# Kernel optimization log

Hardware: AMD Instinct MI355X
Metric: run time of the kernel (lower is better)

The kernel has to match this reference:

```python
import jax, jax.numpy as jnp
import numpy as np

EMBED_DIM = 768
ATTN_DIM = 64


def setup_inputs() -> dict:
    key = jax.random.key(0)
    k1, k2, k3, k4 = jax.random.split(key, 4)
    embedded = jax.random.normal(k1, (4, 4096, EMBED_DIM), dtype=jnp.float32)
    # nn.Linear(embed, attn, bias=False).weight has shape [attn, embed]; y = x @ W.T
    scale = 1.0 / np.sqrt(EMBED_DIM)
    Wq = jax.random.uniform(k2, (ATTN_DIM, EMBED_DIM), dtype=jnp.float32, minval=-scale, maxval=scale)
    Wk = jax.random.uniform(k3, (ATTN_DIM, EMBED_DIM), dtype=jnp.float32, minval=-scale, maxval=scale)
    Wv = jax.random.uniform(k4, (ATTN_DIM, EMBED_DIM), dtype=jnp.float32, minval=-scale, maxval=scale)
    return {"embedded": embedded, "Wq": Wq, "Wk": Wk, "Wv": Wv}


def reference(embedded, Wq, Wk, Wv):
    # Q, K, V: [b, s, a]
    Q = jnp.einsum('bse,ae->bsa', embedded, Wq)
    K = jnp.einsum('bse,ae->bsa', embedded, Wk)
    V = jnp.einsum('bse,ae->bsa', embedded, Wv)
    attn_dim = K.shape[2]
    scores = jnp.einsum('bqa,bka->bqk', Q, K) / jnp.sqrt(jnp.float32(attn_dim))
    s = scores.shape[1]
    # causal mask: positions above the diagonal get -inf
    causal = jnp.tril(jnp.ones((s, s), dtype=bool))
    scores = jnp.where(causal, scores, -jnp.inf)
    probs = jax.nn.softmax(scores, axis=2)
    out = jnp.einsum('bqk,bka->bqa', probs, V)
    return jnp.round(out, 4)
```

## Files before the change

kernel.cpp:

```cpp
#include <hip/hip_runtime.h>
#include <hip/hip_bf16.h>
#include <math.h>

#define EMBED  768
#define SEQ    4096
#define ADIM   64
#define NBATCH 4
#define WELEMS (ADIM * EMBED)
#define QSCALE (0.125f * 1.44269504088896340736f)

typedef __bf16 bf16;
typedef unsigned int u32;
typedef __attribute__((ext_vector_type(8))) __bf16 bf16x8;
typedef __attribute__((ext_vector_type(4))) __bf16 bf16x4;
typedef __attribute__((ext_vector_type(4))) float f32x4;
typedef __attribute__((ext_vector_type(16))) float f32x16;

__device__ __forceinline__ f32x4 mfma16(bf16x8 a, bf16x8 b, f32x4 c) {
  return __builtin_amdgcn_mfma_f32_16x16x32_bf16(a, b, c, 0, 0, 0);
}
__device__ __forceinline__ f32x16 mfma32(bf16x8 a, bf16x8 b, f32x16 c) {
  return __builtin_amdgcn_mfma_f32_32x32x16_bf16(a, b, c, 0, 0, 0);
}
__device__ __forceinline__ unsigned cvtpk(float lo, float hi) {
  unsigned d;
  asm("v_cvt_pk_bf16_f32 %0, %1, %2" : "=v"(d) : "v"(lo), "v"(hi));
  return d;
}
__device__ __forceinline__ void gl_lds16(const bf16* g, bf16* l) {
  __builtin_amdgcn_global_load_lds(
      (const __attribute__((address_space(1))) u32*)g,
      (__attribute__((address_space(3))) u32*)l, 16, 0, 0);
}

__global__ __launch_bounds__(256) void wconv_kernel(
    const float* __restrict__ Wq, const float* __restrict__ Wk,
    const float* __restrict__ Wv, bf16* __restrict__ Wb)
{
  const int gid = blockIdx.x * 256 + threadIdx.x;
  const int m   = gid / (WELEMS / 4);
  const int off = (gid % (WELEMS / 4)) * 4;
  const float* src = (m == 0) ? Wq : ((m == 1) ? Wk : Wv);
  const float  sc  = (m == 0) ? QSCALE : 1.0f;
  float4 v = *reinterpret_cast<const float4*>(src + off);
  bf16x4 o;
  o[0] = (bf16)(v.x * sc); o[1] = (bf16)(v.y * sc);
  o[2] = (bf16)(v.z * sc); o[3] = (bf16)(v.w * sc);
  *reinterpret_cast<bf16x4*>(Wb + (size_t)m * WELEMS + off) = o;
}

__global__ __launch_bounds__(256, 4) void proj_kernel(
    const float* __restrict__ x, const bf16* __restrict__ Wb,
    bf16* __restrict__ Qs, bf16* __restrict__ Ks, bf16* __restrict__ Vt)
{
  __shared__ bf16 Wl[2][192][40];
  __shared__ bf16 Xl[2][32][40];

  const int t    = threadIdx.x;
  const int lane = t & 63;
  const int w    = t >> 6;
  const int band = w >> 1;
  const int half = w & 1;
  const int r    = lane & 15;
  const int g    = lane >> 4;
  const long long row0 = (long long)blockIdx.x * 32;

  f32x4 acc[6];
  #pragma unroll
  for (int i = 0; i < 6; ++i) acc[i] = f32x4{0.f, 0.f, 0.f, 0.f};

  const int wrow = t >> 2;
  const int wg   = t & 3;
  const bf16* wsrc = Wb + (long long)wrow * EMBED + wg * 8;
  const int xrow = t >> 3;
  const int xcol = (t & 7) * 4;
  const float* xsrc = x + (row0 + xrow) * EMBED + xcol;

  {
    bf16x8 wv0 = *reinterpret_cast<const bf16x8*>(wsrc);
    bf16x8 wv1 = *reinterpret_cast<const bf16x8*>(wsrc + (long long)64 * EMBED);
    bf16x8 wv2 = *reinterpret_cast<const bf16x8*>(wsrc + (long long)128 * EMBED);
    float4 xv  = *reinterpret_cast<const float4*>(xsrc);
    *reinterpret_cast<bf16x8*>(&Wl[0][wrow][wg * 8])       = wv0;
    *reinterpret_cast<bf16x8*>(&Wl[0][64 + wrow][wg * 8])  = wv1;
    *reinterpret_cast<bf16x8*>(&Wl[0][128 + wrow][wg * 8]) = wv2;
    uint2 xp; xp.x = cvtpk(xv.x, xv.y); xp.y = cvtpk(xv.z, xv.w);
    *reinterpret_cast<uint2*>(&Xl[0][xrow][xcol]) = xp;
  }
  float4 xv_n = *reinterpret_cast<const float4*>(xsrc + 32);
  __syncthreads();

  int cur = 0;
  for (int kt = 0; kt < 24; ++kt) {
    bf16x8 wv0, wv1, wv2; float4 xv_n2;
    const bool pfW = kt < 23;
    if (pfW) {
      const int k0n = (kt + 1) * 32;
      wv0 = *reinterpret_cast<const bf16x8*>(wsrc + k0n);
      wv1 = *reinterpret_cast<const bf16x8*>(wsrc + (long long)64 * EMBED + k0n);
      wv2 = *reinterpret_cast<const bf16x8*>(wsrc + (long long)128 * EMBED + k0n);
    }
    if (kt < 22)
      xv_n2 = *reinterpret_cast<const float4*>(xsrc + (kt + 2) * 32);

    bf16x8 af = *reinterpret_cast<const bf16x8*>(&Xl[cur][band * 16 + r][g * 8]);
    #pragma unroll
    for (int i = 0; i < 6; ++i) {
      const int n = half * 6 + i;
      bf16x8 bfrag = *reinterpret_cast<const bf16x8*>(&Wl[cur][n * 16 + r][g * 8]);
      acc[i] = mfma16(af, bfrag, acc[i]);
    }

    if (pfW) {
      *reinterpret_cast<bf16x8*>(&Wl[cur ^ 1][wrow][wg * 8])       = wv0;
      *reinterpret_cast<bf16x8*>(&Wl[cur ^ 1][64 + wrow][wg * 8])  = wv1;
      *reinterpret_cast<bf16x8*>(&Wl[cur ^ 1][128 + wrow][wg * 8]) = wv2;
      uint2 xp; xp.x = cvtpk(xv_n.x, xv_n.y); xp.y = cvtpk(xv_n.z, xv_n.w);
      *reinterpret_cast<uint2*>(&Xl[cur ^ 1][xrow][xcol]) = xp;
    }
    xv_n = xv_n2;
    __syncthreads();
    cur ^= 1;
  }

  const long long rowbase = row0 + band * 16 + g * 4;
  const int bb = (int)(rowbase >> 12);
  const int ss = (int)(rowbase & 4095);
  #pragma unroll
  for (int i = 0; i < 6; ++i) {
    const int gt = half * 6 + i;
    if (gt < 4) {
      #pragma unroll
      for (int j = 0; j < 4; ++j)
        Qs[(rowbase + j) * ADIM + gt * 16 + r] = (bf16)(acc[i][j]);
    } else if (gt < 8) {
      #pragma unroll
      for (int j = 0; j < 4; ++j)
        Ks[(rowbase + j) * ADIM + (gt - 4) * 16 + r] = (bf16)(acc[i][j]);
    } else {
      const int d = (gt - 8) * 16 + r;
      bf16x4 pack;
      pack[0] = (bf16)(acc[i][0]); pack[1] = (bf16)(acc[i][1]);
      pack[2] = (bf16)(acc[i][2]); pack[3] = (bf16)(acc[i][3]);
      *reinterpret_cast<bf16x4*>(
          &Vt[(((long long)bb * 128 + (ss >> 5)) * 64 + d) * 32 + (ss & 31)]) = pack;
    }
  }
}

__global__ __launch_bounds__(768) void attn_kernel(
    const bf16* __restrict__ Qs, const bf16* __restrict__ Ks,
    const bf16* __restrict__ Vt, float* __restrict__ out)
{
  __shared__ bf16 Kst[12][2048];
  __shared__ bf16 Vst[12][2048];
  __shared__ unsigned short OldsU[12][32][72];
  __shared__ float Llds[12][32];

  const int t    = threadIdx.x;
  const int lane = t & 63;
  const int w    = t >> 6;
  const int q    = lane & 31;
  const int h    = lane >> 5;
  const int bi   = blockIdx.x;
  const int b    = bi & 3;
  const int p    = bi >> 2;

  const bf16* Qb = Qs + (long long)b * SEQ * ADIM;
  const bf16* Kb = Ks + (long long)b * SEQ * ADIM;
  const bf16* Vb = Vt + (long long)b * SEQ * ADIM;

  const int Ri = lane >> 3;
  const int ci = lane & 7;
  const bf16* kdma = Kb + (long long)Ri * ADIM + (ci ^ Ri) * 8;
  bf16* kslot = &Kst[w][0];
  const int vd = lane >> 2;
  const int vc = lane & 3;
  const bf16* vdma = Vb + (long long)vd * 32 + ((vc ^ (vd & 3)) * 8);
  bf16* vslot = &Vst[w][0];

  const char* kbase = (const char*)kslot;
  const bf16x8* kfp0 = (const bf16x8*)(kbase + q * 128 + (((0 + h) ^ (q & 7)) << 4));
  const bf16x8* kfp1 = (const bf16x8*)(kbase + q * 128 + (((2 + h) ^ (q & 7)) << 4));
  const bf16x8* kfp2 = (const bf16x8*)(kbase + q * 128 + (((4 + h) ^ (q & 7)) << 4));
  const bf16x8* kfp3 = (const bf16x8*)(kbase + q * 128 + (((6 + h) ^ (q & 7)) << 4));
  const char* vbase = (const char*)vslot;
  const bf16x8* vfp00 = (const bf16x8*)(vbase + q * 64        + (((0 + h) ^ (q & 3)) << 4));
  const bf16x8* vfp01 = (const bf16x8*)(vbase + q * 64        + (((2 + h) ^ (q & 3)) << 4));
  const bf16x8* vfp10 = (const bf16x8*)(vbase + 2048 + q * 64 + (((0 + h) ^ (q & 3)) << 4));
  const bf16x8* vfp11 = (const bf16x8*)(vbase + 2048 + q * 64 + (((2 + h) ^ (q & 3)) << 4));

  #define KDMA(st_)                                                          \
    {                                                                        \
      const bf16* ksrc = kdma + (long long)((st_) * 32) * ADIM;              \
      gl_lds16(ksrc,             kslot);                                     \
      gl_lds16(ksrc +  8 * ADIM, kslot + 512);                               \
      gl_lds16(ksrc + 16 * ADIM, kslot + 1024);                              \
      gl_lds16(ksrc + 24 * ADIM, kslot + 1536);                              \
    }
  #define VDMA(st_)                                                          \
    {                                                                        \
      const bf16* vsrc = vdma + (long long)(st_) * 2048;                     \
      gl_lds16(vsrc,        vslot);                                          \
      gl_lds16(vsrc +  512, vslot + 512);                                    \
      gl_lds16(vsrc + 1024, vslot + 1024);                                   \
      gl_lds16(vsrc + 1536, vslot + 1536);                                   \
    }

  for (int ti = 0; ti < 2; ++ti) {
    const int qt = ti ? (127 - p) : p;
    const int qb = qt * 32;

    bf16x8 qf[4];
    #pragma unroll
    for (int kc = 0; kc < 4; ++kc)
      qf[kc] = *reinterpret_cast<const bf16x8*>(Qb + (qb + q) * ADIM + kc * 16 + h * 8);
    __builtin_amdgcn_sched_barrier(0);
    if (w <= qt) { KDMA(w); VDMA(w); }
    __builtin_amdgcn_sched_barrier(0);

    f32x16 o0 = {0,0,0,0,0,0,0,0,0,0,0,0,0,0,0,0};
    f32x16 o1 = {0,0,0,0,0,0,0,0,0,0,0,0,0,0,0,0};
    float l = 0.f;

    for (int st = w; st <= qt; st += 12) {
      const int kv0 = st * 32;
      const bool pf = (st + 12 <= qt);

      asm volatile("s_waitcnt vmcnt(4)" ::: "memory");
      __builtin_amdgcn_sched_barrier(0);
      bf16x8 kf0 = *kfp0, kf1 = *kfp1, kf2 = *kfp2, kf3 = *kfp3;
      asm volatile("s_waitcnt lgkmcnt(0)" ::: "memory");
      __builtin_amdgcn_sched_barrier(0);
      if (pf) KDMA(st + 12);
      __builtin_amdgcn_sched_barrier(0);

      f32x16 s = {0,0,0,0,0,0,0,0,0,0,0,0,0,0,0,0};
      __builtin_amdgcn_s_setprio(1);
      s = mfma32(kf0, qf[0], s);
      s = mfma32(kf1, qf[1], s);
      s = mfma32(kf2, qf[2], s);
      s = mfma32(kf3, qf[3], s);
      __builtin_amdgcn_s_setprio(0);
      __builtin_amdgcn_sched_barrier(0);

      if (pf) { asm volatile("s_waitcnt vmcnt(4)" ::: "memory"); }
      else    { asm volatile("s_waitcnt vmcnt(0)" ::: "memory"); }
      __builtin_amdgcn_sched_barrier(0);
      bf16x8 vf00 = *vfp00, vf01 = *vfp01, vf10 = *vfp10, vf11 = *vfp11;
      asm volatile("s_waitcnt lgkmcnt(0)" ::: "memory");
      __builtin_amdgcn_sched_barrier(0);
      if (pf) VDMA(st + 12);
      __builtin_amdgcn_sched_barrier(0);

      if (st == qt) {
        #pragma unroll
        for (int i = 0; i < 4; ++i)
          #pragma unroll
          for (int j = 0; j < 4; ++j)
            if (kv0 + j + 8 * i + 4 * h > qb + q) s[i * 4 + j] = -INFINITY;
      }

      float rs = 0.f;
      #pragma unroll
      for (int rr = 0; rr < 16; ++rr) { s[rr] = exp2f(s[rr]); rs += s[rr]; }
      l += rs;

      {
        unsigned a0 = cvtpk(s[0], s[1]), a1 = cvtpk(s[2], s[3]);
        unsigned b0 = cvtpk(s[4], s[5]), b1 = cvtpk(s[6], s[7]);
        unsigned a0x = __shfl_xor((int)a0, 32), a1x = __shfl_xor((int)a1, 32);
        unsigned b0x = __shfl_xor((int)b0, 32), b1x = __shfl_xor((int)b1, 32);
        union { unsigned u[4]; bf16x8 v; } pa0;
        pa0.u[0] = h ? b0x : a0;  pa0.u[1] = h ? b1x : a1;
        pa0.u[2] = h ? b0  : a0x; pa0.u[3] = h ? b1  : a1x;
        __builtin_amdgcn_s_setprio(1);
        o0 = mfma32(vf00, pa0.v, o0);
        o1 = mfma32(vf10, pa0.v, o1);
        __builtin_amdgcn_s_setprio(0);
      }
      {
        unsigned c0 = cvtpk(s[8],  s[9]),  c1 = cvtpk(s[10], s[11]);
        unsigned d0 = cvtpk(s[12], s[13]), d1 = cvtpk(s[14], s[15]);
        unsigned c0x = __shfl_xor((int)c0, 32), c1x = __shfl_xor((int)c1, 32);
        unsigned d0x = __shfl_xor((int)d0, 32), d1x = __shfl_xor((int)d1, 32);
        union { unsigned u[4]; bf16x8 v; } pa1;
        pa1.u[0] = h ? d0x : c0;  pa1.u[1] = h ? d1x : c1;
        pa1.u[2] = h ? d0  : c0x; pa1.u[3] = h ? d1  : c1x;
        __builtin_amdgcn_s_setprio(1);
        o0 = mfma32(vf01, pa1.v, o0);
        o1 = mfma32(vf11, pa1.v, o1);
        __builtin_amdgcn_s_setprio(0);
      }
    }

    #pragma unroll
    for (int r2 = 0; r2 < 4; ++r2) {
      uint2 u0, u1;
      u0.x = cvtpk(o0[r2*4+0], o0[r2*4+1]); u0.y = cvtpk(o0[r2*4+2], o0[r2*4+3]);
      u1.x = cvtpk(o1[r2*4+0], o1[r2*4+1]); u1.y = cvtpk(o1[r2*4+2], o1[r2*4+3]);
      *reinterpret_cast<uint2*>(&OldsU[w][q][8 * r2 + 4 * h])      = u0;
      *reinterpret_cast<uint2*>(&OldsU[w][q][32 + 8 * r2 + 4 * h]) = u1;
    }
    const float lt = l + __shfl_xor(l, 32);
    if (h == 0) Llds[w][q] = lt;
    __syncthreads();

    if (t < 512) {
      const int cq = t >> 4;
      const int cd = (t & 15) * 4;
      float lf = 0.f;
      float o4[4] = {0.f, 0.f, 0.f, 0.f};
      #pragma unroll
      for (int w2 = 0; w2 < 12; ++w2) {
        lf += Llds[w2][cq];
        const uint2 uv = *reinterpret_cast<const uint2*>(&OldsU[w2][cq][cd]);
        o4[0] += __uint_as_float(uv.x << 16);
        o4[1] += __uint_as_float(uv.x & 0xffff0000u);
        o4[2] += __uint_as_float(uv.y << 16);
        o4[3] += __uint_as_float(uv.y & 0xffff0000u);
      }
      const float inv = 1.f / lf;
      float4 res;
      res.x = o4[0] * inv; res.y = o4[1] * inv;
      res.z = o4[2] * inv; res.w = o4[3] * inv;
      *reinterpret_cast<float4*>(out + ((long long)b * SEQ + qb + cq) * ADIM + cd) = res;
    }
    __syncthreads();
  }
  #undef KDMA
  #undef VDMA
}

extern "C" void kernel_launch(void* const* d_in, const int* in_sizes, int n_in,
                              void* d_out, int out_size, void* d_ws, size_t ws_size,
                              hipStream_t stream) {
  const float* x  = (const float*)d_in[0];
  const float* Wq = (const float*)d_in[1];
  const float* Wk = (const float*)d_in[2];
  const float* Wv = (const float*)d_in[3];

  const size_t qkvElems = (size_t)NBATCH * SEQ * ADIM;
  bf16* Qs = (bf16*)d_ws;
  bf16* Ks = Qs + qkvElems;
  bf16* Vt = Ks + qkvElems;
  bf16* Wb = Vt + qkvElems;

  wconv_kernel<<<3 * WELEMS / 4 / 256, 256, 0, stream>>>(Wq, Wk, Wv, Wb);
  proj_kernel<<<NBATCH * SEQ / 32, 256, 0, stream>>>(x, Wb, Qs, Ks, Vt);
  attn_kernel<<<256, 768, 0, stream>>>(Qs, Ks, Vt, (float*)d_out);
}
```

Before: 49.80 us.

## Fuse weight conversion, projection and attention into one cooperative kernel

Merges the three launches (weight conversion, QKV projection, attention) into a single cooperative kernel with 256 blocks of 768 threads, separated by a grid-wide sync. The projection now converts fp32 weights to bf16 on the fly and covers 64 rows per block with 12 waves, so the separate weight buffer and two launch gaps are removed. In exchange each block re-converts the full weight matrices, the projection phase runs with only 256 blocks instead of 512 smaller ones, and the grid barrier plus cooperative launch add overhead.

```diff
diff --git a/kernel.cpp b/kernel.cpp
--- a/kernel.cpp
+++ b/kernel.cpp
@@ -1,12 +1,14 @@
 #include <hip/hip_runtime.h>
 #include <hip/hip_bf16.h>
+#include <hip/hip_cooperative_groups.h>
 #include <math.h>
+
+namespace cg = cooperative_groups;
 
 #define EMBED  768
 #define SEQ    4096
 #define ADIM   64
 #define NBATCH 4
-#define WELEMS (ADIM * EMBED)
 #define QSCALE (0.125f * 1.44269504088896340736f)
 
 typedef __bf16 bf16;
@@ -33,303 +35,314 @@
       (__attribute__((address_space(3))) u32*)l, 16, 0, 0);
 }
 
-__global__ __launch_bounds__(256) void wconv_kernel(
+struct ProjLds {
+  bf16 Wl[2][192][40];
+  bf16 Xl[2][64][40];
+};
+struct AttnLds {
+  bf16 Kst[12][2048];
+  bf16 Vst[12][2048];
+  unsigned short OldsU[12][32][72];
+  float Llds[12][32];
+};
+
+__global__ __launch_bounds__(768, 3) void fused_kernel(
+    const float* __restrict__ x,
     const float* __restrict__ Wq, const float* __restrict__ Wk,
-    const float* __restrict__ Wv, bf16* __restrict__ Wb)
+    const float* __restrict__ Wv,
+    bf16* __restrict__ Qs, bf16* __restrict__ Ks, bf16* __restrict__ Vt,
+    float* __restrict__ out)
 {
-  const int gid = blockIdx.x * 256 + threadIdx.x;
-  const int m   = gid / (WELEMS / 4);
-  const int off = (gid % (WELEMS / 4)) * 4;
-  const float* src = (m == 0) ? Wq : ((m == 1) ? Wk : Wv);
-  const float  sc  = (m == 0) ? QSCALE : 1.0f;
-  float4 v = *reinterpret_cast<const float4*>(src + off);
-  bf16x4 o;
-  o[0] = (bf16)(v.x * sc); o[1] = (bf16)(v.y * sc);
-  o[2] = (bf16)(v.z * sc); o[3] = (bf16)(v.w * sc);
-  *reinterpret_cast<bf16x4*>(Wb + (size_t)m * WELEMS + off) = o;
-}
-
-__global__ __launch_bounds__(256, 4) void proj_kernel(
-    const float* __restrict__ x, const bf16* __restrict__ Wb,
-    bf16* __restrict__ Qs, bf16* __restrict__ Ks, bf16* __restrict__ Vt)
-{
-  __shared__ bf16 Wl[2][192][40];
-  __shared__ bf16 Xl[2][32][40];
+  __shared__ alignas(16) char smem[sizeof(AttnLds)];
 
   const int t    = threadIdx.x;
   const int lane = t & 63;
   const int w    = t >> 6;
-  const int band = w >> 1;
-  const int half = w & 1;
   const int r    = lane & 15;
   const int g    = lane >> 4;
-  const long long row0 = (long long)blockIdx.x * 32;
-
-  f32x4 acc[6];
-  #pragma unroll
-  for (int i = 0; i < 6; ++i) acc[i] = f32x4{0.f, 0.f, 0.f, 0.f};
-
-  const int wrow = t >> 2;
-  const int wg   = t & 3;
-  const bf16* wsrc = Wb + (long long)wrow * EMBED + wg * 8;
-  const int xrow = t >> 3;
-  const int xcol = (t & 7) * 4;
-  const float* xsrc = x + (row0 + xrow) * EMBED + xcol;
+  const int bi   = blockIdx.x;
 
   {
-    bf16x8 wv0 = *reinterpret_cast<const bf16x8*>(wsrc);
-    bf16x8 wv1 = *reinterpret_cast<const bf16x8*>(wsrc + (long long)64 * EMBED);
-    bf16x8 wv2 = *reinterpret_cast<const bf16x8*>(wsrc + (long long)128 * EMBED);
-    float4 xv  = *reinterpret_cast<const float4*>(xsrc);
-    *reinterpret_cast<bf16x8*>(&Wl[0][wrow][wg * 8])       = wv0;
-    *reinterpret_cast<bf16x8*>(&Wl[0][64 + wrow][wg * 8])  = wv1;
-    *reinterpret_cast<bf16x8*>(&Wl[0][128 + wrow][wg * 8]) = wv2;
-    uint2 xp; xp.x = cvtpk(xv.x, xv.y); xp.y = cvtpk(xv.z, xv.w);
-    *reinterpret_cast<uint2*>(&Xl[0][xrow][xcol]) = xp;
-  }
-  float4 xv_n = *reinterpret_cast<const float4*>(xsrc + 32);
-  __syncthreads();
-
-  int cur = 0;
-  for (int kt = 0; kt < 24; ++kt) {
-    bf16x8 wv0, wv1, wv2; float4 xv_n2;
-    const bool pfW = kt < 23;
-    if (pfW) {
-      const int k0n = (kt + 1) * 32;
-      wv0 = *reinterpret_cast<const bf16x8*>(wsrc + k0n);
-      wv1 = *reinterpret_cast<const bf16x8*>(wsrc + (long long)64 * EMBED + k0n);
-      wv2 = *reinterpret_cast<const bf16x8*>(wsrc + (long long)128 * EMBED + k0n);
+    ProjLds* P = reinterpret_cast<ProjLds*>(smem);
+    const long long row0 = (long long)bi * 64;
+
+    const int third = w >> 2;
+    const int band  = w & 3;
+
+    f32x4 acc[4];
+    #pragma unroll
+    for (int i = 0; i < 4; ++i) acc[i] = f32x4{0.f, 0.f, 0.f, 0.f};
+
+    const int wrow = t >> 2;
+    const int wm   = wrow >> 6;
+    const float* wsrc = ((wm == 0) ? Wq : (wm == 1) ? Wk : Wv)
+                        + (long long)(wrow & 63) * EMBED + (t & 3) * 8;
+    const float wsc = (wm == 0) ? QSCALE : 1.0f;
+    const int xrow = t >> 3;
+    const int xcol = (t & 7) * 4;
+    const float* xsrc = x + (row0 + xrow) * EMBED + xcol;
+
+    #define STAGE(k0, buf)                                                   \
+      {                                                                      \
+        float4 wa = *reinterpret_cast<const float4*>(wsrc + (k0));           \
+        float4 wb = *reinterpret_cast<const float4*>(wsrc + (k0) + 4);       \
+        uint2 wp0, wp1;                                                      \
+        wp0.x = cvtpk(wa.x * wsc, wa.y * wsc);                               \
+        wp0.y = cvtpk(wa.z * wsc, wa.w * wsc);                               \
+        wp1.x = cvtpk(wb.x * wsc, wb.y * wsc);                               \
+        wp1.y = cvtpk(wb.z * wsc, wb.w * wsc);                               \
+        *reinterpret_cast<uint2*>(&P->Wl[buf][wrow][(t & 3) * 8])     = wp0; \
+        *reinterpret_cast<uint2*>(&P->Wl[buf][wrow][(t & 3) * 8 + 4]) = wp1; \
+        if (t < 512) {                                                       \
+          float4 xv = *reinterpret_cast<const float4*>(xsrc + (k0));         \
+          uint2 xp;                                                          \
+          xp.x = cvtpk(xv.x, xv.y); xp.y = cvtpk(xv.z, xv.w);                \
+          *reinterpret_cast<uint2*>(&P->Xl[buf][xrow][xcol]) = xp;           \
+        }                                                                    \
+      }
+
+    STAGE(0, 0);
+    __syncthreads();
+
+    int cur = 0;
+    for (int kt = 0; kt < 24; ++kt) {
+      float4 wa2, wb2, xv2;
+      const bool pf = kt < 23;
+      if (pf) {
+        const int k0n = (kt + 1) * 32;
+        wa2 = *reinterpret_cast<const float4*>(wsrc + k0n);
+        wb2 = *reinterpret_cast<const float4*>(wsrc + k0n + 4);
+        if (t < 512) xv2 = *reinterpret_cast<const float4*>(xsrc + k0n);
+      }
+
+      bf16x8 af = *reinterpret_cast<const bf16x8*>(&P->Xl[cur][band * 16 + r][g * 8]);
+      #pragma unroll
+      for (int i = 0; i < 4; ++i) {
+        const int n = third * 4 + i;
+        bf16x8 bfrag = *reinterpret_cast<const bf16x8*>(&P->Wl[cur][n * 16 + r][g * 8]);
+        acc[i] = mfma16(af, bfrag, acc[i]);
+      }
+
+      if (pf) {
+        uint2 wp0, wp1;
+        wp0.x = cvtpk(wa2.x * wsc, wa2.y * wsc);
+        wp0.y = cvtpk(wa2.z * wsc, wa2.w * wsc);
+        wp1.x = cvtpk(wb2.x * wsc, wb2.y * wsc);
+        wp1.y = cvtpk(wb2.z * wsc, wb2.w * wsc);
+        *reinterpret_cast<uint2*>(&P->Wl[cur ^ 1][wrow][(t & 3) * 8])     = wp0;
+        *reinterpret_cast<uint2*>(&P->Wl[cur ^ 1][wrow][(t & 3) * 8 + 4]) = wp1;
+        if (t < 512) {
+          uint2 xp; xp.x = cvtpk(xv2.x, xv2.y); xp.y = cvtpk(xv2.z, xv2.w);
+          *reinterpret_cast<uint2*>(&P->Xl[cur ^ 1][xrow][xcol]) = xp;
+        }
+      }
+      __syncthreads();
+      cur ^= 1;
     }
-    if (kt < 22)
-      xv_n2 = *reinterpret_cast<const float4*>(xsrc + (kt + 2) * 32);
-
-    bf16x8 af = *reinterpret_cast<const bf16x8*>(&Xl[cur][band * 16 + r][g * 8]);
-    #pragma unroll
-    for (int i = 0; i < 6; ++i) {
-      const int n = half * 6 + i;
-      bf16x8 bfrag = *reinterpret_cast<const bf16x8*>(&Wl[cur][n * 16 + r][g * 8]);
-      acc[i] = mfma16(af, bfrag, acc[i]);
-    }
-
-    if (pfW) {
-      *reinterpret_cast<bf16x8*>(&Wl[cur ^ 1][wrow][wg * 8])       = wv0;
-      *reinterpret_cast<bf16x8*>(&Wl[cur ^ 1][64 + wrow][wg * 8])  = wv1;
-      *reinterpret_cast<bf16x8*>(&Wl[cur ^ 1][128 + wrow][wg * 8]) = wv2;
-      uint2 xp; xp.x = cvtpk(xv_n.x, xv_n.y); xp.y = cvtpk(xv_n.z, xv_n.w);
-      *reinterpret_cast<uint2*>(&Xl[cur ^ 1][xrow][xcol]) = xp;
-    }
-    xv_n = xv_n2;
-    __syncthreads();
-    cur ^= 1;
-  }
-
-  const long long rowbase = row0 + band * 16 + g * 4;
-  const int bb = (int)(rowbase >> 12);
-  const int ss = (int)(rowbase & 4095);
-  #pragma unroll
-  for (int i = 0; i < 6; ++i) {
-    const int gt = half * 6 + i;
-    if (gt < 4) {
-      #pragma unroll
-      for (int j = 0; j < 4; ++j)
-        Qs[(rowbase + j) * ADIM + gt * 16 + r] = (bf16)(acc[i][j]);
-    } else if (gt < 8) {
-      #pragma unroll
-      for (int j = 0; j < 4; ++j)
-        Ks[(rowbase + j) * ADIM + (gt - 4) * 16 + r] = (bf16)(acc[i][j]);
+    #undef STAGE
+
+    const long long rowbase = row0 + band * 16 + g * 4;
+    const int bb = (int)(rowbase >> 12);
+    const int ss = (int)(rowbase & 4095);
+    if (third == 0) {
+      #pragma unroll
+      for (int i = 0; i < 4; ++i)
+        #pragma unroll
+        for (int j = 0; j < 4; ++j)
+          Qs[(rowbase + j) * ADIM + i * 16 + r] = (bf16)(acc[i][j]);
+    } else if (third == 1) {
+      #pragma unroll
+      for (int i = 0; i < 4; ++i)
+        #pragma unroll
+        for (int j = 0; j < 4; ++j)
+          Ks[(rowbase + j) * ADIM + i * 16 + r] = (bf16)(acc[i][j]);
     } else {
-      const int d = (gt - 8) * 16 + r;
-      bf16x4 pack;
-      pack[0] = (bf16)(acc[i][0]); pack[1] = (bf16)(acc[i][1]);
-      pack[2] = (bf16)(acc[i][2]); pack[3] = (bf16)(acc[i][3]);
-      *reinterpret_cast<bf16x4*>(
-          &Vt[(((long long)bb * 128 + (ss >> 5)) * 64 + d) * 32 + (ss & 31)]) = pack;
+      #pragma unroll
+      for (int i = 0; i < 4; ++i) {
+        const int d = i * 16 + r;
+        bf16x4 pack;
+        pack[0] = (bf16)(acc[i][0]); pack[1] = (bf16)(acc[i][1]);
+        pack[2] = (bf16)(acc[i][2]); pack[3] = (bf16)(acc[i][3]);
+        *reinterpret_cast<bf16x4*>(
+            &Vt[(((long long)bb * 128 + (ss >> 5)) * 64 + d) * 32 + (ss & 31)]) = pack;
+      }
     }
   }
-}
-
-__global__ __launch_bounds__(768) void attn_kernel(
-    const bf16* __restrict__ Qs, const bf16* __restrict__ Ks,
-    const bf16* __restrict__ Vt, float* __restrict__ out)
-{
-  __shared__ bf16 Kst[12][2048];
-  __shared__ bf16 Vst[12][2048];
-  __shared__ unsigned short OldsU[12][32][72];
-  __shared__ float Llds[12][32];
-
-  const int t    = threadIdx.x;
-  const int lane = t & 63;
-  const int w    = t >> 6;
-  const int q    = lane & 31;
-  const int h    = lane >> 5;
-  const int bi   = blockIdx.x;
-  const int b    = bi & 3;
-  const int p    = bi >> 2;
-
-  const bf16* Qb = Qs + (long long)b * SEQ * ADIM;
-  const bf16* Kb = Ks + (long long)b * SEQ * ADIM;
-  const bf16* Vb = Vt + (long long)b * SEQ * ADIM;
-
-  const int Ri = lane >> 3;
-  const int ci = lane & 7;
-  const bf16* kdma = Kb + (long long)Ri * ADIM + (ci ^ Ri) * 8;
-  bf16* kslot = &Kst[w][0];
-  const int vd = lane >> 2;
-  const int vc = lane & 3;
-  const bf16* vdma = Vb + (long long)vd * 32 + ((vc ^ (vd & 3)) * 8);
-  bf16* vslot = &Vst[w][0];
-
-  const char* kbase = (const char*)kslot;
-  const bf16x8* kfp0 = (const bf16x8*)(kbase + q * 128 + (((0 + h) ^ (q & 7)) << 4));
-  const bf16x8* kfp1 = (const bf16x8*)(kbase + q * 128 + (((2 + h) ^ (q & 7)) << 4));
-  const bf16x8* kfp2 = (const bf16x8*)(kbase + q * 128 + (((4 + h) ^ (q & 7)) << 4));
-  const bf16x8* kfp3 = (const bf16x8*)(kbase + q * 128 + (((6 + h) ^ (q & 7)) << 4));
-  const char* vbase = (const char*)vslot;
-  const bf16x8* vfp00 = (const bf16x8*)(vbase + q * 64        + (((0 + h) ^ (q & 3)) << 4));
-  const bf16x8* vfp01 = (const bf16x8*)(vbase + q * 64        + (((2 + h) ^ (q & 3)) << 4));
-  const bf16x8* vfp10 = (const bf16x8*)(vbase + 2048 + q * 64 + (((0 + h) ^ (q & 3)) << 4));
-  const bf16x8* vfp11 = (const bf16x8*)(vbase + 2048 + q * 64 + (((2 + h) ^ (q & 3)) << 4));
-
-  #define KDMA(st_)                                                          \
-    {                                                                        \
-      const bf16* ksrc = kdma + (long long)((st_) * 32) * ADIM;              \
-      gl_lds16(ksrc,             kslot);                                     \
-      gl_lds16(ksrc +  8 * ADIM, kslot + 512);                               \
-      gl_lds16(ksrc + 16 * ADIM, kslot + 1024);                              \
-      gl_lds16(ksrc + 24 * ADIM, kslot + 1536);                              \
+
+  cg::this_grid().sync();
+
+  {
+    AttnLds* A = reinterpret_cast<AttnLds*>(smem);
+    const int q = lane & 31;
+    const int h = lane >> 5;
+    const int b = bi & 3;
+    const int p = bi >> 2;
+
+    const bf16* Qb = Qs + (long long)b * SEQ * ADIM;
+    const bf16* Kb = Ks + (long long)b * SEQ * ADIM;
+    const bf16* Vb = Vt + (long long)b * SEQ * ADIM;
+
+    const int Ri = lane >> 3;
+    const int ci = lane & 7;
+    const bf16* kdma = Kb + (long long)Ri * ADIM + (ci ^ Ri) * 8;
+    bf16* kslot = &A->Kst[w][0];
+    const int vd = lane >> 2;
+    const int vc = lane & 3;
+    const bf16* vdma = Vb + (long long)vd * 32 + ((vc ^ (vd & 3)) * 8);
+    bf16* vslot = &A->Vst[w][0];
+
+    const char* kbase = (const char*)kslot;
+    const bf16x8* kfp0 = (const bf16x8*)(kbase + q * 128 + (((0 + h) ^ (q & 7)) << 4));
+    const bf16x8* kfp1 = (const bf16x8*)(kbase + q * 128 + (((2 + h) ^ (q & 7)) << 4));
+    const bf16x8* kfp2 = (const bf16x8*)(kbase + q * 128 + (((4 + h) ^ (q & 7)) << 4));
+    const bf16x8* kfp3 = (const bf16x8*)(kbase + q * 128 + (((6 + h) ^ (q & 7)) << 4));
+    const char* vbase = (const char*)vslot;
+    const bf16x8* vfp00 = (const bf16x8*)(vbase + q * 64        + (((0 + h) ^ (q & 3)) << 4));
+    const bf16x8* vfp01 = (const bf16x8*)(vbase + q * 64        + (((2 + h) ^ (q & 3)) << 4));
+    const bf16x8* vfp10 = (const bf16x8*)(vbase + 2048 + q * 64 + (((0 + h) ^ (q & 3)) << 4));
+    const bf16x8* vfp11 = (const bf16x8*)(vbase + 2048 + q * 64 + (((2 + h) ^ (q & 3)) << 4));
+
+    #define KDMA(st_)                                                        \
+      {                                                                      \
+        const bf16* ksrc = kdma + (long long)((st_) * 32) * ADIM;            \
+        gl_lds16(ksrc,             kslot);                                   \
+        gl_lds16(ksrc +  8 * ADIM, kslot + 512);                             \
+        gl_lds16(ksrc + 16 * ADIM, kslot + 1024);                            \
+        gl_lds16(ksrc + 24 * ADIM, kslot + 1536);                            \
+      }
+    #define VDMA(st_)                                                        \
+      {                                                                      \
+        const bf16* vsrc = vdma + (long long)(st_) * 2048;                   \
+        gl_lds16(vsrc,        vslot);                                        \
+        gl_lds16(vsrc +  512, vslot + 512);                                  \
+        gl_lds16(vsrc + 1024, vslot + 1024);                                 \
+        gl_lds16(vsrc + 1536, vslot + 1536);                                 \
+      }
+
+    for (int ti = 0; ti < 2; ++ti) {
+      const int qt = ti ? (127 - p) : p;
+      const int qb = qt * 32;
+
+      bf16x8 qf[4];
+      #pragma unroll
+      for (int kc = 0; kc < 4; ++kc)
+        qf[kc] = *reinterpret_cast<const bf16x8*>(Qb + (qb + q) * ADIM + kc * 16 + h * 8);
+      __builtin_amdgcn_sched_barrier(0);
+      if (w <= qt) { KDMA(w); VDMA(w); }
+      __builtin_amdgcn_sched_barrier(0);
+
+      f32x16 o0 = {0,0,0,0,0,0,0,0,0,0,0,0,0,0,0,0};
+      f32x16 o1 = {0,0,0,0,0,0,0,0,0,0,0,0,0,0,0,0};
+      float l = 0.f;
+
+      for (int st = w; st <= qt; st += 12) {
+        const int kv0 = st * 32;
+        const bool pf = (st + 12 <= qt);
+
+        asm volatile("s_waitcnt vmcnt(4)" ::: "memory");
+        __builtin_amdgcn_sched_barrier(0);
+        bf16x8 kf0 = *kfp0, kf1 = *kfp1, kf2 = *kfp2, kf3 = *kfp3;
+        asm volatile("s_waitcnt lgkmcnt(0)" ::: "memory");
+        __builtin_amdgcn_sched_barrier(0);
+        if (pf) KDMA(st + 12);
+        __builtin_amdgcn_sched_barrier(0);
+
+        f32x16 s = {0,0,0,0,0,0,0,0,0,0,0,0,0,0,0,0};
+        __builtin_amdgcn_s_setprio(1);
+        s = mfma32(kf0, qf[0], s);
+        s = mfma32(kf1, qf[1], s);
+        s = mfma32(kf2, qf[2], s);
+        s = mfma32(kf3, qf[3], s);
+        __builtin_amdgcn_s_setprio(0);
+        __builtin_amdgcn_sched_barrier(0);
+
+        if (pf) { asm volatile("s_waitcnt vmcnt(4)" ::: "memory"); }
+        else    { asm volatile("s_waitcnt vmcnt(0)" ::: "memory"); }
+        __builtin_amdgcn_sched_barrier(0);
+        bf16x8 vf00 = *vfp00, vf01 = *vfp01, vf10 = *vfp10, vf11 = *vfp11;
+        asm volatile("s_waitcnt lgkmcnt(0)" ::: "memory");
+        __builtin_amdgcn_sched_barrier(0);
+        if (pf) VDMA(st + 12);
+        __builtin_amdgcn_sched_barrier(0);
+
+        if (st == qt) {
+          #pragma unroll
+          for (int i = 0; i < 4; ++i)
+            #pragma unroll
+            for (int j = 0; j < 4; ++j)
+              if (kv0 + j + 8 * i + 4 * h > qb + q) s[i * 4 + j] = -INFINITY;
+        }
+
+        float rs = 0.f;
+        #pragma unroll
+        for (int rr = 0; rr < 16; ++rr) { s[rr] = exp2f(s[rr]); rs += s[rr]; }
+        l += rs;
+
+        {
+          unsigned a0 = cvtpk(s[0], s[1]), a1 = cvtpk(s[2], s[3]);
+          unsigned b0 = cvtpk(s[4], s[5]), b1 = cvtpk(s[6], s[7]);
+          unsigned a0x = __shfl_xor((int)a0, 32), a1x = __shfl_xor((int)a1, 32);
+          unsigned b0x = __shfl_xor((int)b0, 32), b1x = __shfl_xor((int)b1, 32);
+          union { unsigned u[4]; bf16x8 v; } pa0;
+          pa0.u[0] = h ? b0x : a0;  pa0.u[1] = h ? b1x : a1;
+          pa0.u[2] = h ? b0  : a0x; pa0.u[3] = h ? b1  : a1x;
+          __builtin_amdgcn_s_setprio(1);
+          o0 = mfma32(vf00, pa0.v, o0);
+          o1 = mfma32(vf10, pa0.v, o1);
+          __builtin_amdgcn_s_setprio(0);
+        }
+        {
+          unsigned c0 = cvtpk(s[8],  s[9]),  c1 = cvtpk(s[10], s[11]);
+          unsigned d0 = cvtpk(s[12], s[13]), d1 = cvtpk(s[14], s[15]);
+          unsigned c0x = __shfl_xor((int)c0, 32), c1x = __shfl_xor((int)c1, 32);
+          unsigned d0x = __shfl_xor((int)d0, 32), d1x = __shfl_xor((int)d1, 32);
+          union { unsigned u[4]; bf16x8 v; } pa1;
+          pa1.u[0] = h ? d0x : c0;  pa1.u[1] = h ? d1x : c1;
+          pa1.u[2] = h ? d0  : c0x; pa1.u[3] = h ? d1  : c1x;
+          __builtin_amdgcn_s_setprio(1);
+          o0 = mfma32(vf01, pa1.v, o0);
+          o1 = mfma32(vf11, pa1.v, o1);
+          __builtin_amdgcn_s_setprio(0);
+        }
+      }
+
+      #pragma unroll
+      for (int r2 = 0; r2 < 4; ++r2) {
+        uint2 u0, u1;
+        u0.x = cvtpk(o0[r2*4+0], o0[r2*4+1]); u0.y = cvtpk(o0[r2*4+2], o0[r2*4+3]);
+        u1.x = cvtpk(o1[r2*4+0], o1[r2*4+1]); u1.y = cvtpk(o1[r2*4+2], o1[r2*4+3]);
+        *reinterpret_cast<uint2*>(&A->OldsU[w][q][8 * r2 + 4 * h])      = u0;
+        *reinterpret_cast<uint2*>(&A->OldsU[w][q][32 + 8 * r2 + 4 * h]) = u1;
+      }
+      const float lt = l + __shfl_xor(l, 32);
+      if (h == 0) A->Llds[w][q] = lt;
+      __syncthreads();
+
+      if (t < 512) {
+        const int cq = t >> 4;
+        const int cd = (t & 15) * 4;
+        float lf = 0.f;
+        float o4[4] = {0.f, 0.f, 0.f, 0.f};
+        #pragma unroll
+        for (int w2 = 0; w2 < 12; ++w2) {
+          lf += A->Llds[w2][cq];
+          const uint2 uv = *reinterpret_cast<const uint2*>(&A->OldsU[w2][cq][cd]);
+          o4[0] += __uint_as_float(uv.x << 16);
+          o4[1] += __uint_as_float(uv.x & 0xffff0000u);
+          o4[2] += __uint_as_float(uv.y << 16);
+          o4[3] += __uint_as_float(uv.y & 0xffff0000u);
+        }
+        const float inv = 1.f / lf;
+        float4 res;
+        res.x = o4[0] * inv; res.y = o4[1] * inv;
+        res.z = o4[2] * inv; res.w = o4[3] * inv;
+        *reinterpret_cast<float4*>(out + ((long long)b * SEQ + qb + cq) * ADIM + cd) = res;
+      }
+      __syncthreads();
     }
-  #define VDMA(st_)                                                          \
-    {                                                                        \
-      const bf16* vsrc = vdma + (long long)(st_) * 2048;                     \
-      gl_lds16(vsrc,        vslot);                                          \
-      gl_lds16(vsrc +  512, vslot + 512);                                    \
-      gl_lds16(vsrc + 1024, vslot + 1024);                                   \
-      gl_lds16(vsrc + 1536, vslot + 1536);                                   \
-    }
-
-  for (int ti = 0; ti < 2; ++ti) {
-    const int qt = ti ? (127 - p) : p;
-    const int qb = qt * 32;
-
-    bf16x8 qf[4];
-    #pragma unroll
-    for (int kc = 0; kc < 4; ++kc)
-      qf[kc] = *reinterpret_cast<const bf16x8*>(Qb + (qb + q) * ADIM + kc * 16 + h * 8);
-    __builtin_amdgcn_sched_barrier(0);
-    if (w <= qt) { KDMA(w); VDMA(w); }
-    __builtin_amdgcn_sched_barrier(0);
-
-    f32x16 o0 = {0,0,0,0,0,0,0,0,0,0,0,0,0,0,0,0};
-    f32x16 o1 = {0,0,0,0,0,0,0,0,0,0,0,0,0,0,0,0};
-    float l = 0.f;
-
-    for (int st = w; st <= qt; st += 12) {
-      const int kv0 = st * 32;
-      const bool pf = (st + 12 <= qt);
-
-      asm volatile("s_waitcnt vmcnt(4)" ::: "memory");
-      __builtin_amdgcn_sched_barrier(0);
-      bf16x8 kf0 = *kfp0, kf1 = *kfp1, kf2 = *kfp2, kf3 = *kfp3;
-      asm volatile("s_waitcnt lgkmcnt(0)" ::: "memory");
-      __builtin_amdgcn_sched_barrier(0);
-      if (pf) KDMA(st + 12);
-      __builtin_amdgcn_sched_barrier(0);
-
-      f32x16 s = {0,0,0,0,0,0,0,0,0,0,0,0,0,0,0,0};
-      __builtin_amdgcn_s_setprio(1);
-      s = mfma32(kf0, qf[0], s);
-      s = mfma32(kf1, qf[1], s);
-      s = mfma32(kf2, qf[2], s);
-      s = mfma32(kf3, qf[3], s);
-      __builtin_amdgcn_s_setprio(0);
-      __builtin_amdgcn_sched_barrier(0);
-
-      if (pf) { asm volatile("s_waitcnt vmcnt(4)" ::: "memory"); }
-      else    { asm volatile("s_waitcnt vmcnt(0)" ::: "memory"); }
-      __builtin_amdgcn_sched_barrier(0);
-      bf16x8 vf00 = *vfp00, vf01 = *vfp01, vf10 = *vfp10, vf11 = *vfp11;
-      asm volatile("s_waitcnt lgkmcnt(0)" ::: "memory");
-      __builtin_amdgcn_sched_barrier(0);
-      if (pf) VDMA(st + 12);
-      __builtin_amdgcn_sched_barrier(0);
-
-      if (st == qt) {
-        #pragma unroll
-        for (int i = 0; i < 4; ++i)
-          #pragma unroll
-          for (int j = 0; j < 4; ++j)
-            if (kv0 + j + 8 * i + 4 * h > qb + q) s[i * 4 + j] = -INFINITY;
-      }
-
-      float rs = 0.f;
-      #pragma unroll
-      for (int rr = 0; rr < 16; ++rr) { s[rr] = exp2f(s[rr]); rs += s[rr]; }
-      l += rs;
-
-      {
-        unsigned a0 = cvtpk(s[0], s[1]), a1 = cvtpk(s[2], s[3]);
-        unsigned b0 = cvtpk(s[4], s[5]), b1 = cvtpk(s[6], s[7]);
-        unsigned a0x = __shfl_xor((int)a0, 32), a1x = __shfl_xor((int)a1, 32);
-        unsigned b0x = __shfl_xor((int)b0, 32), b1x = __shfl_xor((int)b1, 32);
-        union { unsigned u[4]; bf16x8 v; } pa0;
-        pa0.u[0] = h ? b0x : a0;  pa0.u[1] = h ? b1x : a1;
-        pa0.u[2] = h ? b0  : a0x; pa0.u[3] = h ? b1  : a1x;
-        __builtin_amdgcn_s_setprio(1);
-        o0 = mfma32(vf00, pa0.v, o0);
-        o1 = mfma32(vf10, pa0.v, o1);
-        __builtin_amdgcn_s_setprio(0);
-      }
-      {
-        unsigned c0 = cvtpk(s[8],  s[9]),  c1 = cvtpk(s[10], s[11]);
-        unsigned d0 = cvtpk(s[12], s[13]), d1 = cvtpk(s[14], s[15]);
-        unsigned c0x = __shfl_xor((int)c0, 32), c1x = __shfl_xor((int)c1, 32);
-        unsigned d0x = __shfl_xor((int)d0, 32), d1x = __shfl_xor((int)d1, 32);
-        union { unsigned u[4]; bf16x8 v; } pa1;
-        pa1.u[0] = h ? d0x : c0;  pa1.u[1] = h ? d1x : c1;
-        pa1.u[2] = h ? d0  : c0x; pa1.u[3] = h ? d1  : c1x;
-        __builtin_amdgcn_s_setprio(1);
-        o0 = mfma32(vf01, pa1.v, o0);
-        o1 = mfma32(vf11, pa1.v, o1);
-        __builtin_amdgcn_s_setprio(0);
-      }
-    }
-
-    #pragma unroll
-    for (int r2 = 0; r2 < 4; ++r2) {
-      uint2 u0, u1;
-      u0.x = cvtpk(o0[r2*4+0], o0[r2*4+1]); u0.y = cvtpk(o0[r2*4+2], o0[r2*4+3]);
-      u1.x = cvtpk(o1[r2*4+0], o1[r2*4+1]); u1.y = cvtpk(o1[r2*4+2], o1[r2*4+3]);
-      *reinterpret_cast<uint2*>(&OldsU[w][q][8 * r2 + 4 * h])      = u0;
-      *reinterpret_cast<uint2*>(&OldsU[w][q][32 + 8 * r2 + 4 * h]) = u1;
-    }
-    const float lt = l + __shfl_xor(l, 32);
-    if (h == 0) Llds[w][q] = lt;
-    __syncthreads();
-
-    if (t < 512) {
-      const int cq = t >> 4;
-      const int cd = (t & 15) * 4;
-      float lf = 0.f;
-      float o4[4] = {0.f, 0.f, 0.f, 0.f};
-      #pragma unroll
-      for (int w2 = 0; w2 < 12; ++w2) {
-        lf += Llds[w2][cq];
-        const uint2 uv = *reinterpret_cast<const uint2*>(&OldsU[w2][cq][cd]);
-        o4[0] += __uint_as_float(uv.x << 16);
-        o4[1] += __uint_as_float(uv.x & 0xffff0000u);
-        o4[2] += __uint_as_float(uv.y << 16);
-        o4[3] += __uint_as_float(uv.y & 0xffff0000u);
-      }
-      const float inv = 1.f / lf;
-      float4 res;
-      res.x = o4[0] * inv; res.y = o4[1] * inv;
-      res.z = o4[2] * inv; res.w = o4[3] * inv;
-      *reinterpret_cast<float4*>(out + ((long long)b * SEQ + qb + cq) * ADIM + cd) = res;
-    }
-    __syncthreads();
+    #undef KDMA
+    #undef VDMA
   }
-  #undef KDMA
-  #undef VDMA
 }
 
 extern "C" void kernel_launch(void* const* d_in, const int* in_sizes, int n_in,
@@ -344,9 +357,10 @@
   bf16* Qs = (bf16*)d_ws;
   bf16* Ks = Qs + qkvElems;
   bf16* Vt = Ks + qkvElems;
-  bf16* Wb = Vt + qkvElems;
-
-  wconv_kernel<<<3 * WELEMS / 4 / 256, 256, 0, stream>>>(Wq, Wk, Wv, Wb);
-  proj_kernel<<<NBATCH * SEQ / 32, 256, 0, stream>>>(x, Wb, Qs, Ks, Vt);
-  attn_kernel<<<256, 768, 0, stream>>>(Qs, Ks, Vt, (float*)d_out);
-}
+  float* out = (float*)d_out;
+
+  void* args[] = {(void*)&x, (void*)&Wq, (void*)&Wk, (void*)&Wv,
+                  (void*)&Qs, (void*)&Ks, (void*)&Vt, (void*)&out};
+  hipLaunchCooperativeKernel((void*)fused_kernel, dim3(256), dim3(768),
+                             args, 0, stream);
+}
```

Result: slower. 95.76 us (+92.3%).
